# Optimization experiments

Hardware: AMD Instinct MI355X
Metric: run time of the kernel (lower is better)

Reference implementation:

```python
import jax, jax.numpy as jnp
import numpy as np


def _normalized_adj(A):
    # get_a: d = 0.5*I, a = off-diagonal ones + A, a2 = d @ a @ d
    off = jnp.array([[0., 1., 1.], [1., 0., 1.], [1., 1., 0.]], dtype=A.dtype)
    a = off + A
    d = 0.5 * jnp.eye(3, dtype=A.dtype)
    return d @ a @ d  # [3,3]


def setup_inputs() -> dict:
    key = jax.random.key(0)
    k1, k2 = jax.random.split(key)
    B = 8192
    x = jax.random.normal(k1, (B, 3, 10), dtype=jnp.float32)
    A = jnp.eye(3, dtype=jnp.float32)  # get_A() returns identity; Parameter init
    stdv = 1.0 / np.sqrt(10.0)
    W = jax.random.uniform(k2, (10, 10), dtype=jnp.float32, minval=-stdv, maxval=stdv)
    return {"x": x, "A": A, "W": W}


def reference(x, A, W):
    # adjacency is detached in the torch forward
    adj = jax.lax.stop_gradient(_normalized_adj(A))  # [3,3], shared across batch
    # GraphConvolution: adj @ (x @ W)
    support = jnp.einsum('bnf,fo->bno', x, W)          # [B,3,10]
    h = jnp.einsum('nm,bmo->bno', adj, support)        # [B,3,10]
    # permute -> [B,10,3]; AvgPool1d(2) on length 3 -> length 1: mean of nodes 0,1
    pooled = 0.5 * (h[:, 0, :] + h[:, 1, :])           # [B,10]
    # ScaleDotProductAttention over the batch axis
    score = jax.nn.softmax(pooled @ pooled.T, axis=-1)  # [B,B]
    v = score @ pooled                                  # [B,10]
    return v
```

## Files before the change

kernel.cpp:

```cpp
#include <hip/hip_runtime.h>
#include <math.h>

#define BROWS 8192
#define F 10
#define TJ 512
#define QP 20
#define AP 520
#define NT (BROWS / TJ)
#define LOG2E 1.44269504088896340736f

#if __has_builtin(__builtin_amdgcn_exp2f)
#define EXP2F(x) __builtin_amdgcn_exp2f(x)
#else
#define EXP2F(x) exp2f(x)
#endif

typedef _Float16 half4 __attribute__((ext_vector_type(4)));
typedef __fp16 fp16x2 __attribute__((ext_vector_type(2)));
typedef float floatx4 __attribute__((ext_vector_type(4)));

__device__ __forceinline__ half4 exp4_to_h4(float a, float b, float c, float d) {
#if __has_builtin(__builtin_amdgcn_cvt_pkrtz)
    union { fp16x2 h2[2]; half4 h4; } u;
    u.h2[0] = __builtin_amdgcn_cvt_pkrtz(EXP2F(a), EXP2F(b));
    u.h2[1] = __builtin_amdgcn_cvt_pkrtz(EXP2F(c), EXP2F(d));
    return u.h4;
#else
    half4 r;
    r[0] = (_Float16)EXP2F(a); r[1] = (_Float16)EXP2F(b);
    r[2] = (_Float16)EXP2F(c); r[3] = (_Float16)EXP2F(d);
    return r;
#endif
}

__device__ __forceinline__ uint32_t pack2(_Float16 a, _Float16 b) {
    union { _Float16 h[2]; uint32_t u; } x;
    x.h[0] = a; x.h[1] = b;
    return x.u;
}

__device__ __forceinline__ void gload_lds16(const void* g, void* l) {
#if __has_builtin(__builtin_amdgcn_global_load_lds)
    __builtin_amdgcn_global_load_lds(
        (const __attribute__((address_space(1))) void*)g,
        (__attribute__((address_space(3))) void*)l, 16, 0, 0);
#else
    *(float4*)l = *(const float4*)g;
#endif
}

__global__ void pooled_kernel(const float* __restrict__ x,
                              const float* __restrict__ A,
                              const float* __restrict__ W,
                              _Float16* __restrict__ poolQ,
                              _Float16* __restrict__ poolT) {
    int b = blockIdx.x * blockDim.x + threadIdx.x;
    if (b >= BROWS) return;

    float c0 = 0.125f * (1.0f + A[0] + A[3]);
    float c1 = 0.125f * (1.0f + A[1] + A[4]);
    float c2 = 0.125f * (2.0f + A[2] + A[5]);

    const float2* xb = (const float2*)(x + (size_t)b * 3 * F);
    float xv[3 * F];
#pragma unroll
    for (int k = 0; k < 15; ++k) {
        float2 t = xb[k];
        xv[2 * k] = t.x; xv[2 * k + 1] = t.y;
    }

    float y[F];
#pragma unroll
    for (int f = 0; f < F; ++f)
        y[f] = c0 * xv[f] + c1 * xv[F + f] + c2 * xv[2 * F + f];

    float po[F];
#pragma unroll
    for (int o = 0; o < F; ++o) {
        float acc = 0.0f;
#pragma unroll
        for (int f = 0; f < F; ++f)
            acc = fmaf(y[f], W[f * F + o], acc);
        po[o] = acc;
    }

    uint2* qd = (uint2*)(poolQ + (size_t)b * QP);
    qd[0] = make_uint2(pack2((_Float16)po[0], (_Float16)po[1]),
                       pack2((_Float16)po[2], (_Float16)po[3]));
    qd[1] = make_uint2(pack2((_Float16)po[4], (_Float16)po[5]),
                       pack2((_Float16)po[6], (_Float16)po[7]));
    qd[2] = make_uint2(pack2((_Float16)po[8], (_Float16)po[9]), 0u);
    qd[3] = make_uint2(0u, 0u);
    qd[4] = make_uint2(0u, 0u);

#pragma unroll
    for (int o = 0; o < F; ++o)
        poolT[(size_t)o * BROWS + b] = (_Float16)po[o];
}

__global__ void attn_kernel(const _Float16* __restrict__ poolQ,
                            const _Float16* __restrict__ poolT,
                            float* __restrict__ out) {
    __shared__ __align__(16) _Float16 qbuf[2][TJ * QP];
    __shared__ __align__(16) _Float16 abuf[2][16 * AP];
    __shared__ __align__(16) float red[8 * 16 * 12];

    const int tid  = threadIdx.x;
    const int wave = tid >> 6;
    const int lane = tid & 63;
    const int m    = lane & 15;
    const int quad = lane >> 4;
    const int irow = blockIdx.x * 16 + m;

    half4 b1;
#pragma unroll
    for (int idx = 0; idx < 4; ++idx) {
        int f = quad * 4 + idx;
        float v = (f < F) ? (float)poolQ[(size_t)irow * QP + f] * LOG2E : 0.0f;
        b1[idx] = (_Float16)v;
    }

    for (int e = tid; e < 2 * 6 * AP; e += 512) {
        int bufi = e / (6 * AP);
        int r    = e % (6 * AP);
        int n    = 10 + r / AP;
        int j    = r % AP;
        abuf[bufi][n * AP + j] = (n == 10) ? (_Float16)1.0f : (_Float16)0.0f;
    }

    auto dma_tile = [&](int t, int bufi) {
        const char* qs = (const char*)poolQ + (size_t)t * TJ * QP * 2;
        char* qd = (char*)&qbuf[bufi][0];
        for (int d = wave; d < 20; d += 8)
            gload_lds16(qs + d * 1024 + lane * 16, qd + d * 1024 + lane * 16);
        char* ad = (char*)&abuf[bufi][0];
        for (int n = wave; n < F; n += 8)
            gload_lds16((const char*)(poolT + (size_t)n * BROWS + t * TJ) + lane * 16,
                        ad + n * (AP * 2) + lane * 16);
    };

    floatx4 acc0 = {0.f, 0.f, 0.f, 0.f};
    floatx4 acc1 = {0.f, 0.f, 0.f, 0.f};

    dma_tile(0, 0);
    __syncthreads();

    for (int t = 0; t < NT; ++t) {
        const int buf = t & 1;
        if (t + 1 < NT) dma_tile(t + 1, buf ^ 1);

#pragma unroll
        for (int c = 0; c < 4; ++c) {
            const int jb = wave * 64 + c * 16;
            half4 a1 = *(const half4*)&qbuf[buf][(jb + m) * QP + quad * 4];
            floatx4 d1 = __builtin_amdgcn_mfma_f32_16x16x16f16(
                a1, b1, (floatx4){0.f, 0.f, 0.f, 0.f}, 0, 0, 0);
            half4 a2 = exp4_to_h4(d1[0], d1[1], d1[2], d1[3]);
            half4 ag = *(const half4*)&abuf[buf][m * AP + jb + quad * 4];
            if (c & 1)
                acc1 = __builtin_amdgcn_mfma_f32_16x16x16f16(ag, a2, acc1, 0, 0, 0);
            else
                acc0 = __builtin_amdgcn_mfma_f32_16x16x16f16(ag, a2, acc0, 0, 0, 0);
        }
        __syncthreads();
    }

    floatx4 acc = acc0 + acc1;

    if (quad < 3)
        *(floatx4*)&red[(wave * 16 + m) * 12 + quad * 4] = acc;
    __syncthreads();

    if (tid < 160) {
        const int i16 = tid / 10;
        const int f   = tid % 10;
        float sum = 0.0f, l = 0.0f;
#pragma unroll
        for (int w = 0; w < 8; ++w) {
            sum += red[(w * 16 + i16) * 12 + f];
            l   += red[(w * 16 + i16) * 12 + 10];
        }
        out[(size_t)(blockIdx.x * 16 + i16) * F + f] = sum / l;
    }
}

extern "C" void kernel_launch(void* const* d_in, const int* in_sizes, int n_in,
                              void* d_out, int out_size, void* d_ws, size_t ws_size,
                              hipStream_t stream) {
    const float* x = (const float*)d_in[0];
    const float* A = (const float*)d_in[1];
    const float* W = (const float*)d_in[2];
    float* out = (float*)d_out;

    _Float16* poolQ = (_Float16*)d_ws;
    _Float16* poolT = (_Float16*)((char*)d_ws + 327680);

    pooled_kernel<<<BROWS / 64, 64, 0, stream>>>(x, A, W, poolQ, poolT);
    attn_kernel<<<BROWS / 16, 512, 0, stream>>>(poolQ, poolT, out);
}
```

Baseline: 76.46 us.

## Load attention operands directly from global memory instead of LDS double buffering

Removes the shared-memory staging (global_load_lds double buffers plus per-tile barriers) in the attention kernel, so each lane reads its MFMA operands straight from global/L2. The transposed value matrix is padded to 16 rows by the pooled kernel, which now writes the ones row and the zero rows, so the in-kernel LDS init loop goes away. This removes the barriers and cuts LDS use, which may raise occupancy. The cost is that global load latency is exposed and only covered by the unroll, with small 8-byte strided reads against a heavily shared 330KB working set.

```diff
diff --git a/kernel.cpp b/kernel.cpp
--- a/kernel.cpp
+++ b/kernel.cpp
@@ -3,10 +3,7 @@
 
 #define BROWS 8192
 #define F 10
-#define TJ 512
 #define QP 20
-#define AP 520
-#define NT (BROWS / TJ)
 #define LOG2E 1.44269504088896340736f
 
 #if __has_builtin(__builtin_amdgcn_exp2f)
@@ -39,21 +36,11 @@
     return x.u;
 }
 
-__device__ __forceinline__ void gload_lds16(const void* g, void* l) {
-#if __has_builtin(__builtin_amdgcn_global_load_lds)
-    __builtin_amdgcn_global_load_lds(
-        (const __attribute__((address_space(1))) void*)g,
-        (__attribute__((address_space(3))) void*)l, 16, 0, 0);
-#else
-    *(float4*)l = *(const float4*)g;
-#endif
-}
-
 __global__ void pooled_kernel(const float* __restrict__ x,
                               const float* __restrict__ A,
                               const float* __restrict__ W,
                               _Float16* __restrict__ poolQ,
-                              _Float16* __restrict__ poolT) {
+                              _Float16* __restrict__ poolT16) {
     int b = blockIdx.x * blockDim.x + threadIdx.x;
     if (b >= BROWS) return;
 
@@ -95,14 +82,16 @@
 
 #pragma unroll
     for (int o = 0; o < F; ++o)
-        poolT[(size_t)o * BROWS + b] = (_Float16)po[o];
+        poolT16[(size_t)o * BROWS + b] = (_Float16)po[o];
+    poolT16[(size_t)10 * BROWS + b] = (_Float16)1.0f;
+#pragma unroll
+    for (int o = 11; o < 16; ++o)
+        poolT16[(size_t)o * BROWS + b] = (_Float16)0.0f;
 }
 
 __global__ void attn_kernel(const _Float16* __restrict__ poolQ,
-                            const _Float16* __restrict__ poolT,
+                            const _Float16* __restrict__ poolT16,
                             float* __restrict__ out) {
-    __shared__ __align__(16) _Float16 qbuf[2][TJ * QP];
-    __shared__ __align__(16) _Float16 abuf[2][16 * AP];
     __shared__ __align__(16) float red[8 * 16 * 12];
 
     const int tid  = threadIdx.x;
@@ -120,49 +109,27 @@
         b1[idx] = (_Float16)v;
     }
 
-    for (int e = tid; e < 2 * 6 * AP; e += 512) {
-        int bufi = e / (6 * AP);
-        int r    = e % (6 * AP);
-        int n    = 10 + r / AP;
-        int j    = r % AP;
-        abuf[bufi][n * AP + j] = (n == 10) ? (_Float16)1.0f : (_Float16)0.0f;
-    }
-
-    auto dma_tile = [&](int t, int bufi) {
-        const char* qs = (const char*)poolQ + (size_t)t * TJ * QP * 2;
-        char* qd = (char*)&qbuf[bufi][0];
-        for (int d = wave; d < 20; d += 8)
-            gload_lds16(qs + d * 1024 + lane * 16, qd + d * 1024 + lane * 16);
-        char* ad = (char*)&abuf[bufi][0];
-        for (int n = wave; n < F; n += 8)
-            gload_lds16((const char*)(poolT + (size_t)n * BROWS + t * TJ) + lane * 16,
-                        ad + n * (AP * 2) + lane * 16);
-    };
+    const char* qbase = (const char*)poolQ
+                      + (size_t)(wave * 64 + m) * (QP * 2) + quad * 8;
+    const char* tbase = (const char*)poolT16
+                      + (size_t)m * (BROWS * 2) + (size_t)(wave * 64) * 2 + quad * 8;
 
     floatx4 acc0 = {0.f, 0.f, 0.f, 0.f};
     floatx4 acc1 = {0.f, 0.f, 0.f, 0.f};
 
-    dma_tile(0, 0);
-    __syncthreads();
-
-    for (int t = 0; t < NT; ++t) {
-        const int buf = t & 1;
-        if (t + 1 < NT) dma_tile(t + 1, buf ^ 1);
-
-#pragma unroll
-        for (int c = 0; c < 4; ++c) {
-            const int jb = wave * 64 + c * 16;
-            half4 a1 = *(const half4*)&qbuf[buf][(jb + m) * QP + quad * 4];
-            floatx4 d1 = __builtin_amdgcn_mfma_f32_16x16x16f16(
-                a1, b1, (floatx4){0.f, 0.f, 0.f, 0.f}, 0, 0, 0);
-            half4 a2 = exp4_to_h4(d1[0], d1[1], d1[2], d1[3]);
-            half4 ag = *(const half4*)&abuf[buf][m * AP + jb + quad * 4];
-            if (c & 1)
-                acc1 = __builtin_amdgcn_mfma_f32_16x16x16f16(ag, a2, acc1, 0, 0, 0);
-            else
-                acc0 = __builtin_amdgcn_mfma_f32_16x16x16f16(ag, a2, acc0, 0, 0, 0);
-        }
-        __syncthreads();
+#pragma unroll 8
+    for (int idx = 0; idx < 64; ++idx) {
+        const int t = idx >> 2, c = idx & 3;
+        const int joff = t * 512 + c * 16;
+        half4 a1 = *(const half4*)(qbase + (size_t)joff * (QP * 2));
+        half4 ag = *(const half4*)(tbase + (size_t)joff * 2);
+        floatx4 d1 = __builtin_amdgcn_mfma_f32_16x16x16f16(
+            a1, b1, (floatx4){0.f, 0.f, 0.f, 0.f}, 0, 0, 0);
+        half4 a2 = exp4_to_h4(d1[0], d1[1], d1[2], d1[3]);
+        if (idx & 1)
+            acc1 = __builtin_amdgcn_mfma_f32_16x16x16f16(ag, a2, acc1, 0, 0, 0);
+        else
+            acc0 = __builtin_amdgcn_mfma_f32_16x16x16f16(ag, a2, acc0, 0, 0, 0);
     }
 
     floatx4 acc = acc0 + acc1;
@@ -192,9 +159,9 @@
     const float* W = (const float*)d_in[2];
     float* out = (float*)d_out;
 
-    _Float16* poolQ = (_Float16*)d_ws;
-    _Float16* poolT = (_Float16*)((char*)d_ws + 327680);
+    _Float16* poolQ   = (_Float16*)d_ws;
+    _Float16* poolT16 = (_Float16*)((char*)d_ws + 327680);
 
-    pooled_kernel<<<BROWS / 64, 64, 0, stream>>>(x, A, W, poolQ, poolT);
-    attn_kernel<<<BROWS / 16, 512, 0, stream>>>(poolQ, poolT, out);
+    pooled_kernel<<<BROWS / 64, 64, 0, stream>>>(x, A, W, poolQ, poolT16);
+    attn_kernel<<<BROWS / 16, 512, 0, stream>>>(poolQ, poolT16, out);
 }
```

After: 98.13 us. 1.28x slower.
